# Performance work log

Hardware: AMD Instinct MI355X
Metric: run time of the kernel (lower is better)

Reference implementation:

```python
import jax, jax.numpy as jnp
import numpy as np

N_NODES = 50000


def _sage_conv(x, src, dst, Wl, bl, Wr):
    # mean aggregation of source-node features into target nodes
    agg = jax.ops.segment_sum(x[src], dst, num_segments=N_NODES)      # [N, C]
    deg = jax.ops.segment_sum(jnp.ones_like(src, dtype=x.dtype), dst,
                              num_segments=N_NODES)                   # [N]
    mean = agg / jnp.maximum(deg, 1.0)[:, None]
    # PyG SAGEConv: lin_l(aggr) (with bias) + lin_r(x) (no bias)
    return mean @ Wl.T + bl + x @ Wr.T


def setup_inputs() -> dict:
    key = jax.random.key(0)
    ks = jax.random.split(key, 8)
    C = 128
    E = 600000
    scale = 1.0 / np.sqrt(C)
    x = jax.random.normal(ks[0], (N_NODES, C), dtype=jnp.float32)
    edge_index = jax.random.randint(ks[1], (2, E), 0, N_NODES, dtype=jnp.int64)
    Wl1 = jax.random.normal(ks[2], (C, C), dtype=jnp.float32) * scale
    bl1 = jnp.zeros((C,), dtype=jnp.float32)
    Wr1 = jax.random.normal(ks[3], (C, C), dtype=jnp.float32) * scale
    Wl2 = jax.random.normal(ks[4], (C, C), dtype=jnp.float32) * scale
    bl2 = jnp.zeros((C,), dtype=jnp.float32)
    Wr2 = jax.random.normal(ks[5], (C, C), dtype=jnp.float32) * scale
    return {"x": x, "edge_index": edge_index, "Wl1": Wl1, "bl1": bl1,
            "Wr1": Wr1, "Wl2": Wl2, "bl2": bl2, "Wr2": Wr2}


def reference(x, edge_index, Wl1, bl1, Wr1, Wl2, bl2, Wr2):
    src, dst = edge_index[0], edge_index[1]
    h = _sage_conv(x, src, dst, Wl1, bl1, Wr1)
    h = jax.nn.relu(h)
    out = _sage_conv(h, src, dst, Wl2, bl2, Wr2)
    return out
```

## Files before the change

kernel.cpp:

```cpp
#include <hip/hip_runtime.h>
#include <hip/hip_bf16.h>

#define N_NODES 50000
#define C 128
#define NPAD 50176
#define FUSED_BLOCKS (NPAD / 64)
#define XPREP_BLOCKS 3125
#define WPREP_BLOCKS 256
#define CAP 48
#define CSTRIDE 32
#define FPITCH 132

typedef short bf16x8 __attribute__((ext_vector_type(8)));
typedef float f32x4 __attribute__((ext_vector_type(4)));

__device__ __forceinline__ unsigned short f2bf(float f) {
    unsigned int u = __float_as_uint(f);
    unsigned int r = u + 0x7fffu + ((u >> 16) & 1u);
    return (unsigned short)(r >> 16);
}

__device__ __forceinline__ float bf2f(unsigned short b) {
    return __uint_as_float(((unsigned int)b) << 16);
}

__device__ __forceinline__ void acc8(float* a, uint4 u) {
    const unsigned int uu[4] = {u.x, u.y, u.z, u.w};
#pragma unroll
    for (int i = 0; i < 4; ++i) {
        a[2 * i] += bf2f((unsigned short)uu[i]);
        a[2 * i + 1] += bf2f((unsigned short)(uu[i] >> 16));
    }
}

__global__ __launch_bounds__(256) void buildfill_kernel(
    const int* __restrict__ src, const int* __restrict__ dst, int E, int edgeBlocks,
    int* __restrict__ cursor, int* __restrict__ csr,
    const float* __restrict__ x, unsigned short* __restrict__ Xb,
    const float* __restrict__ Wl1, const float* __restrict__ Wr1,
    const float* __restrict__ Wl2, const float* __restrict__ Wr2,
    unsigned short* __restrict__ Wc1, unsigned short* __restrict__ Wc2) {
    int b = blockIdx.x;
    if (b < edgeBlocks) {
        int e = b * 256 + threadIdx.x;
        if (e < E) {
            int d = dst[e];
            int s = src[e];
            if ((unsigned)d < (unsigned)N_NODES && (unsigned)s < (unsigned)N_NODES) {
                int slot = atomicAdd(cursor + d * CSTRIDE, 1);
                if (slot < CAP) csr[d * CAP + slot] = s;
            }
        }
    } else if (b < edgeBlocks + XPREP_BLOCKS) {
        int t = (b - edgeBlocks) * 256 + threadIdx.x;
        if (t >= N_NODES * C / 8) return;
        const float4 a = *(const float4*)(x + (size_t)t * 8);
        const float4 c = *(const float4*)(x + (size_t)t * 8 + 4);
        unsigned short o[8] = {f2bf(a.x), f2bf(a.y), f2bf(a.z), f2bf(a.w),
                               f2bf(c.x), f2bf(c.y), f2bf(c.z), f2bf(c.w)};
        *(uint4*)(Xb + (size_t)t * 8) = *(const uint4*)o;
    } else {
        int idx = (b - edgeBlocks - XPREP_BLOCKS) * 256 + threadIdx.x;
        int layer = idx >> 15;
        int r = idx & 32767;
        int j = r >> 8, k = r & 255;
        const float* Wl = layer ? Wl2 : Wl1;
        const float* Wr = layer ? Wr2 : Wr1;
        unsigned short* Wc = layer ? Wc2 : Wc1;
        float f = (k < 128) ? Wl[j * 128 + k] : Wr[j * 128 + (k - 128)];
        Wc[r] = f2bf(f);
    }
}

__global__ __launch_bounds__(256, 4) void sage_fused(
    const unsigned short* __restrict__ feat,
    const int* __restrict__ cursor, const int* __restrict__ csr,
    const unsigned short* __restrict__ Wc,
    const float* __restrict__ bias,
    void* __restrict__ outv, int relu, int obf16) {
    __shared__ unsigned short fm[64 * FPITCH];

    const int lane = threadIdx.x & 63;
    const int w = threadIdx.x >> 6;
    const int g = lane >> 4;
    const int c = lane & 15;
    const int base = blockIdx.x * 64;
    const unsigned short* fp = feat + c * 8;

#pragma unroll 1
    for (int i = 0; i < 16; ++i) {
        const int rl = w * 16 + i;
        const int node = base + rl;
        if (node < N_NODES) {
            const int degraw = cursor[(size_t)node * CSTRIDE];
            const int myidx = (lane < CAP) ? csr[node * CAP + lane] : 0;
            const int deg = min(degraw, CAP);
            float a[8];
#pragma unroll
            for (int k = 0; k < 8; ++k) a[k] = 0.f;
            const int nb = (deg + 3) >> 2;
            uint4 u[6];
#pragma unroll
            for (int b = 0; b < 6; ++b) {
                if (b < nb) {
                    int r = 4 * b + g;
                    int s = __shfl(myidx, r < deg ? r : 0);
                    u[b] = *(const uint4*)(fp + (size_t)s * C);
                }
            }
#pragma unroll
            for (int b = 0; b < 6; ++b) {
                if (b < nb && 4 * b + g < deg) acc8(a, u[b]);
            }
            if (nb > 6) {
                for (int b = 6; b < nb; ++b) {
                    int r = 4 * b + g;
                    int s = __shfl(myidx, r < deg ? r : 0);
                    uint4 uu = *(const uint4*)(fp + (size_t)s * C);
                    if (r < deg) acc8(a, uu);
                }
            }
#pragma unroll
            for (int k = 0; k < 8; ++k) {
                a[k] += __shfl_xor(a[k], 16);
                a[k] += __shfl_xor(a[k], 32);
            }
            const float inv = 1.0f / fmaxf((float)deg, 1.0f);
            if (g == 0) {
                unsigned int o[4];
#pragma unroll
                for (int k = 0; k < 4; ++k)
                    o[k] = (unsigned)f2bf(a[2 * k] * inv) |
                           ((unsigned)f2bf(a[2 * k + 1] * inv) << 16);
                *(uint4*)(&fm[rl * FPITCH + c * 8]) = *(const uint4*)o;
            }
        } else if (g == 0) {
            const uint4 z = {0u, 0u, 0u, 0u};
            *(uint4*)(&fm[rl * FPITCH + c * 8]) = z;
        }
    }
    __syncthreads();

    const int m = lane & 15;
    const int q = lane >> 4;
    const unsigned short* as = feat + (size_t)(base + w * 16 + m) * C + q * 8;

    f32x4 acc[8];
#pragma unroll
    for (int j = 0; j < 8; ++j) acc[j] = (f32x4){0.f, 0.f, 0.f, 0.f};

#pragma unroll
    for (int kt = 0; kt < 8; ++kt) {
        bf16x8 af;
        if (kt < 4)
            af = *(const bf16x8*)(&fm[(w * 16 + m) * FPITCH + kt * 32 + q * 8]);
        else
            af = *(const bf16x8*)(as + (kt & 3) * 32);
#pragma unroll
        for (int jt = 0; jt < 8; ++jt) {
            bf16x8 bfrag = *(const bf16x8*)(Wc + (jt * 16 + m) * 256 + kt * 32 + q * 8);
            acc[jt] = __builtin_amdgcn_mfma_f32_16x16x32_bf16(af, bfrag, acc[jt], 0, 0, 0);
        }
    }

    const int rbase = base + w * 16 + q * 4;
#pragma unroll
    for (int r = 0; r < 4; ++r) {
        int row = rbase + r;
        if (row < N_NODES) {
#pragma unroll
            for (int jt = 0; jt < 8; ++jt) {
                int col = jt * 16 + m;
                float v = acc[jt][r] + bias[col];
                if (relu) v = fmaxf(v, 0.0f);
                if (obf16)
                    ((unsigned short*)outv)[(size_t)row * C + col] = f2bf(v);
                else
                    ((float*)outv)[(size_t)row * C + col] = v;
            }
        }
    }
}

extern "C" void kernel_launch(void* const* d_in, const int* in_sizes, int n_in,
                              void* d_out, int out_size, void* d_ws, size_t ws_size,
                              hipStream_t stream) {
    const float* x = (const float*)d_in[0];
    const int* edge = (const int*)d_in[1];
    const float* Wl1 = (const float*)d_in[2];
    const float* bl1 = (const float*)d_in[3];
    const float* Wr1 = (const float*)d_in[4];
    const float* Wl2 = (const float*)d_in[5];
    const float* bl2 = (const float*)d_in[6];
    const float* Wr2 = (const float*)d_in[7];
    float* out = (float*)d_out;

    const int E = in_sizes[1] / 2;
    const int* src = edge;
    const int* dst = edge + E;

    char* ws = (char*)d_ws;
    size_t off = 0;
    int* cursor = (int*)(ws + off);           off += (size_t)N_NODES * CSTRIDE * 4;
    off = (off + 511) & ~511ull;
    int* csr = (int*)(ws + off);              off += (size_t)N_NODES * CAP * 4;
    off = (off + 511) & ~511ull;
    unsigned short* Xb = (unsigned short*)(ws + off); off += (size_t)NPAD * C * 2;
    unsigned short* h  = (unsigned short*)(ws + off); off += (size_t)NPAD * C * 2;
    unsigned short* Wc1 = (unsigned short*)(ws + off); off += 128 * 256 * 2;
    unsigned short* Wc2 = (unsigned short*)(ws + off); off += 128 * 256 * 2;
    (void)ws_size;

    const int edgeBlocks = (E + 255) / 256;

    hipMemsetAsync(cursor, 0, (size_t)N_NODES * CSTRIDE * 4, stream);
    buildfill_kernel<<<edgeBlocks + XPREP_BLOCKS + WPREP_BLOCKS, 256, 0, stream>>>(
        src, dst, E, edgeBlocks, cursor, csr, x, Xb, Wl1, Wr1, Wl2, Wr2, Wc1, Wc2);

    sage_fused<<<FUSED_BLOCKS, 256, 0, stream>>>(Xb, cursor, csr, Wc1, bl1, h, 1, 1);

    sage_fused<<<FUSED_BLOCKS, 256, 0, stream>>>(h, cursor, csr, Wc2, bl2, out, 0, 0);
}
```

Before: 245.8 us.

## Shrink fused SAGE blocks to 16 rows and gather two nodes per pass

Each block now handles 16 nodes instead of 64, giving about four times as many blocks. Each wave aggregates 4 nodes, issuing the neighbor gathers for two nodes together so more independent memory loads are in flight. Only wave 0 runs the 16x128 MFMA projection afterwards, so three of four waves sit idle during the GEMM phase. Each block also reloads the weight matrix, which roughly quadruples weight reads per node, and the bounds checks are dropped because 50000 divides evenly by 16.

```diff
diff --git a/kernel.cpp b/kernel.cpp
--- a/kernel.cpp
+++ b/kernel.cpp
@@ -4,7 +4,8 @@
 #define N_NODES 50000
 #define C 128
 #define NPAD 50176
-#define FUSED_BLOCKS (NPAD / 64)
+#define FB_ROWS 16
+#define FUSED_BLOCKS (N_NODES / FB_ROWS)
 #define XPREP_BLOCKS 3125
 #define WPREP_BLOCKS 256
 #define CAP 48
@@ -72,78 +73,117 @@
     }
 }
 
-__global__ __launch_bounds__(256, 4) void sage_fused(
+__global__ __launch_bounds__(256, 4) void sage_fused16(
     const unsigned short* __restrict__ feat,
     const int* __restrict__ cursor, const int* __restrict__ csr,
     const unsigned short* __restrict__ Wc,
     const float* __restrict__ bias,
     void* __restrict__ outv, int relu, int obf16) {
-    __shared__ unsigned short fm[64 * FPITCH];
+    __shared__ unsigned short fm[FB_ROWS * FPITCH];
 
     const int lane = threadIdx.x & 63;
     const int w = threadIdx.x >> 6;
     const int g = lane >> 4;
     const int c = lane & 15;
-    const int base = blockIdx.x * 64;
+    const int base = blockIdx.x * FB_ROWS;
     const unsigned short* fp = feat + c * 8;
 
-#pragma unroll 1
-    for (int i = 0; i < 16; ++i) {
-        const int rl = w * 16 + i;
-        const int node = base + rl;
-        if (node < N_NODES) {
-            const int degraw = cursor[(size_t)node * CSTRIDE];
-            const int myidx = (lane < CAP) ? csr[node * CAP + lane] : 0;
-            const int deg = min(degraw, CAP);
-            float a[8];
-#pragma unroll
-            for (int k = 0; k < 8; ++k) a[k] = 0.f;
-            const int nb = (deg + 3) >> 2;
-            uint4 u[6];
-#pragma unroll
-            for (int b = 0; b < 6; ++b) {
-                if (b < nb) {
-                    int r = 4 * b + g;
-                    int s = __shfl(myidx, r < deg ? r : 0);
-                    u[b] = *(const uint4*)(fp + (size_t)s * C);
-                }
-            }
-#pragma unroll
-            for (int b = 0; b < 6; ++b) {
-                if (b < nb && 4 * b + g < deg) acc8(a, u[b]);
-            }
-            if (nb > 6) {
-                for (int b = 6; b < nb; ++b) {
-                    int r = 4 * b + g;
-                    int s = __shfl(myidx, r < deg ? r : 0);
-                    uint4 uu = *(const uint4*)(fp + (size_t)s * C);
-                    if (r < deg) acc8(a, uu);
-                }
-            }
-#pragma unroll
-            for (int k = 0; k < 8; ++k) {
-                a[k] += __shfl_xor(a[k], 16);
-                a[k] += __shfl_xor(a[k], 32);
-            }
-            const float inv = 1.0f / fmaxf((float)deg, 1.0f);
+    const int n0 = base + w * 4;
+    int degr[4], idx[4];
+#pragma unroll
+    for (int i = 0; i < 4; ++i) degr[i] = cursor[(size_t)(n0 + i) * CSTRIDE];
+#pragma unroll
+    for (int i = 0; i < 4; ++i) idx[i] = (lane < CAP) ? csr[(n0 + i) * CAP + lane] : 0;
+
+#pragma unroll
+    for (int p = 0; p < 2; ++p) {
+        const int d0 = min(degr[2 * p], CAP);
+        const int d1 = min(degr[2 * p + 1], CAP);
+        const int i0 = idx[2 * p], i1 = idx[2 * p + 1];
+        const int nb0 = (d0 + 3) >> 2, nb1 = (d1 + 3) >> 2;
+        uint4 u0[6], u1[6];
+#pragma unroll
+        for (int b = 0; b < 6; ++b) {
+            if (b < nb0) {
+                int r = 4 * b + g;
+                int s = __shfl(i0, r < d0 ? r : 0);
+                u0[b] = *(const uint4*)(fp + (size_t)s * C);
+            }
+        }
+#pragma unroll
+        for (int b = 0; b < 6; ++b) {
+            if (b < nb1) {
+                int r = 4 * b + g;
+                int s = __shfl(i1, r < d1 ? r : 0);
+                u1[b] = *(const uint4*)(fp + (size_t)s * C);
+            }
+        }
+        float a[8];
+#pragma unroll
+        for (int k = 0; k < 8; ++k) a[k] = 0.f;
+#pragma unroll
+        for (int b = 0; b < 6; ++b)
+            if (b < nb0 && 4 * b + g < d0) acc8(a, u0[b]);
+        if (nb0 > 6) {
+            for (int b = 6; b < nb0; ++b) {
+                int r = 4 * b + g;
+                int s = __shfl(i0, r < d0 ? r : 0);
+                uint4 uu = *(const uint4*)(fp + (size_t)s * C);
+                if (r < d0) acc8(a, uu);
+            }
+        }
+#pragma unroll
+        for (int k = 0; k < 8; ++k) {
+            a[k] += __shfl_xor(a[k], 16);
+            a[k] += __shfl_xor(a[k], 32);
+        }
+        {
+            const float inv = 1.0f / fmaxf((float)d0, 1.0f);
             if (g == 0) {
                 unsigned int o[4];
 #pragma unroll
                 for (int k = 0; k < 4; ++k)
                     o[k] = (unsigned)f2bf(a[2 * k] * inv) |
                            ((unsigned)f2bf(a[2 * k + 1] * inv) << 16);
-                *(uint4*)(&fm[rl * FPITCH + c * 8]) = *(const uint4*)o;
-            }
-        } else if (g == 0) {
-            const uint4 z = {0u, 0u, 0u, 0u};
-            *(uint4*)(&fm[rl * FPITCH + c * 8]) = z;
+                *(uint4*)(&fm[(w * 4 + 2 * p) * FPITCH + c * 8]) = *(const uint4*)o;
+            }
+        }
+#pragma unroll
+        for (int k = 0; k < 8; ++k) a[k] = 0.f;
+#pragma unroll
+        for (int b = 0; b < 6; ++b)
+            if (b < nb1 && 4 * b + g < d1) acc8(a, u1[b]);
+        if (nb1 > 6) {
+            for (int b = 6; b < nb1; ++b) {
+                int r = 4 * b + g;
+                int s = __shfl(i1, r < d1 ? r : 0);
+                uint4 uu = *(const uint4*)(fp + (size_t)s * C);
+                if (r < d1) acc8(a, uu);
+            }
+        }
+#pragma unroll
+        for (int k = 0; k < 8; ++k) {
+            a[k] += __shfl_xor(a[k], 16);
+            a[k] += __shfl_xor(a[k], 32);
+        }
+        {
+            const float inv = 1.0f / fmaxf((float)d1, 1.0f);
+            if (g == 0) {
+                unsigned int o[4];
+#pragma unroll
+                for (int k = 0; k < 4; ++k)
+                    o[k] = (unsigned)f2bf(a[2 * k] * inv) |
+                           ((unsigned)f2bf(a[2 * k + 1] * inv) << 16);
+                *(uint4*)(&fm[(w * 4 + 2 * p + 1) * FPITCH + c * 8]) = *(const uint4*)o;
+            }
         }
     }
     __syncthreads();
 
+    if (w != 0) return;
     const int m = lane & 15;
     const int q = lane >> 4;
-    const unsigned short* as = feat + (size_t)(base + w * 16 + m) * C + q * 8;
+    const unsigned short* as = feat + (size_t)(base + m) * C + q * 8;
 
     f32x4 acc[8];
 #pragma unroll
@@ -153,7 +193,7 @@
     for (int kt = 0; kt < 8; ++kt) {
         bf16x8 af;
         if (kt < 4)
-            af = *(const bf16x8*)(&fm[(w * 16 + m) * FPITCH + kt * 32 + q * 8]);
+            af = *(const bf16x8*)(&fm[m * FPITCH + kt * 32 + q * 8]);
         else
             af = *(const bf16x8*)(as + (kt & 3) * 32);
 #pragma unroll
@@ -163,21 +203,19 @@
         }
     }
 
-    const int rbase = base + w * 16 + q * 4;
+    const int rbase = base + q * 4;
 #pragma unroll
     for (int r = 0; r < 4; ++r) {
         int row = rbase + r;
-        if (row < N_NODES) {
-#pragma unroll
-            for (int jt = 0; jt < 8; ++jt) {
-                int col = jt * 16 + m;
-                float v = acc[jt][r] + bias[col];
-                if (relu) v = fmaxf(v, 0.0f);
-                if (obf16)
-                    ((unsigned short*)outv)[(size_t)row * C + col] = f2bf(v);
-                else
-                    ((float*)outv)[(size_t)row * C + col] = v;
-            }
+#pragma unroll
+        for (int jt = 0; jt < 8; ++jt) {
+            int col = jt * 16 + m;
+            float v = acc[jt][r] + bias[col];
+            if (relu) v = fmaxf(v, 0.0f);
+            if (obf16)
+                ((unsigned short*)outv)[(size_t)row * C + col] = f2bf(v);
+            else
+                ((float*)outv)[(size_t)row * C + col] = v;
         }
     }
 }
@@ -217,7 +255,7 @@
     buildfill_kernel<<<edgeBlocks + XPREP_BLOCKS + WPREP_BLOCKS, 256, 0, stream>>>(
         src, dst, E, edgeBlocks, cursor, csr, x, Xb, Wl1, Wr1, Wl2, Wr2, Wc1, Wc2);
 
-    sage_fused<<<FUSED_BLOCKS, 256, 0, stream>>>(Xb, cursor, csr, Wc1, bl1, h, 1, 1);
-
-    sage_fused<<<FUSED_BLOCKS, 256, 0, stream>>>(h, cursor, csr, Wc2, bl2, out, 0, 0);
-}
+    sage_fused16<<<FUSED_BLOCKS, 256, 0, stream>>>(Xb, cursor, csr, Wc1, bl1, h, 1, 1);
+
+    sage_fused16<<<FUSED_BLOCKS, 256, 0, stream>>>(h, cursor, csr, Wc2, bl2, out, 0, 0);
+}
```

After: 209.8 us. 14.6% less time.
